# Kernel optimization log

Hardware: AMD Instinct MI355X
Metric: run time of the kernel (lower is better)

Reference implementation:

```python
import jax, jax.numpy as jnp
import numpy as np

H = 16
D_MODEL = 1024
D_K = D_MODEL // H


def setup_inputs() -> dict:
    key = jax.random.key(0)
    ks = jax.random.split(key, 12)
    B, S = 2, 2048
    scale = 1.0 / np.sqrt(D_MODEL)
    inp = {
        "query": jax.random.normal(ks[0], (B, S, D_MODEL), jnp.float32),
        "key": jax.random.normal(ks[1], (B, S, D_MODEL), jnp.float32),
        "value": jax.random.normal(ks[2], (B, S, D_MODEL), jnp.float32),
        "mask": jax.random.randint(ks[3], (B, S, S), 0, 2, jnp.int32),
        "w_q": jax.random.normal(ks[4], (D_MODEL, D_MODEL), jnp.float32) * scale,
        "b_q": jnp.zeros((D_MODEL,), jnp.float32),
        "w_k": jax.random.normal(ks[5], (D_MODEL, D_MODEL), jnp.float32) * scale,
        "b_k": jnp.zeros((D_MODEL,), jnp.float32),
        "w_v": jax.random.normal(ks[6], (D_MODEL, D_MODEL), jnp.float32) * scale,
        "b_v": jnp.zeros((D_MODEL,), jnp.float32),
        "w_o": jax.random.normal(ks[7], (D_MODEL, D_MODEL), jnp.float32) * scale,
        "b_o": jnp.zeros((D_MODEL,), jnp.float32),
    }
    return inp


def reference(query, key, value, mask, w_q, b_q, w_k, b_k, w_v, b_v, w_o, b_o):
    B, S, _ = query.shape
    # linear projections (torch nn.Linear: x @ W^T + b)
    q = query @ w_q.T + b_q
    k = key @ w_k.T + b_k
    v = value @ w_v.T + b_v
    # split heads -> [B, H, S, D_K]
    q = q.reshape(B, S, H, D_K).transpose(0, 2, 1, 3)
    k = k.reshape(B, S, H, D_K).transpose(0, 2, 1, 3)
    v = v.reshape(B, S, H, D_K).transpose(0, 2, 1, 3)
    # scores [B, H, S, S]; original masks BEFORE dividing by sqrt(d_k)
    scores = jnp.einsum("bhqd,bhkd->bhqk", q, k)
    m = mask[:, None, :, :]  # broadcast over heads (mask.unsqueeze(1))
    scores = jnp.where(m == 0, jnp.float32(-1e9), scores)
    scores = scores / jnp.sqrt(jnp.float32(D_K))
    attn = jax.nn.softmax(scores, axis=-1)
    # dropout is identity in eval mode
    ctx = jnp.einsum("bhqk,bhkd->bhqd", attn, v)
    ctx = ctx.transpose(0, 2, 1, 3).reshape(B, S, H * D_K)
    return ctx @ w_o.T + b_o
```

## Files before the change

kernel.cpp:

```cpp
#include <hip/hip_runtime.h>
#include <hip/hip_bf16.h>
#include <stdint.h>

typedef __attribute__((ext_vector_type(8))) short short8;
typedef __attribute__((ext_vector_type(4))) short short4v;
typedef __attribute__((ext_vector_type(4))) float f32x4;
typedef __attribute__((ext_vector_type(4))) unsigned short us4;
typedef unsigned short ushort_t;

#define LDS_AS __attribute__((address_space(3)))
#define GLB_AS __attribute__((address_space(1)))

__device__ __forceinline__ void gload_lds16(const void* g, void* l) {
    __builtin_amdgcn_global_load_lds((const GLB_AS uint32_t*)g, (LDS_AS uint32_t*)l, 16, 0, 0);
}

__device__ __forceinline__ unsigned short f2bf(float f) {
    union { float f; uint32_t u; } v; v.f = f;
    uint32_t r = v.u + 0x7FFFu + ((v.u >> 16) & 1u);
    return (unsigned short)(r >> 16);
}

__device__ __forceinline__ float fexp2(float x) {
#if __has_builtin(__builtin_amdgcn_exp2f)
    return __builtin_amdgcn_exp2f(x);
#else
    return exp2f(x);
#endif
}

__device__ __forceinline__ uint32_t fbits(float f) {
    union { float f; uint32_t u; } v; v.f = f; return v.u;
}

__device__ __forceinline__ f32x4 mfma32(short8 a, short8 b, f32x4 c) {
    return __builtin_amdgcn_mfma_f32_16x16x32_bf16(a, b, c, 0, 0, 0);
}
__device__ __forceinline__ f32x4 mfma16(short4v a, short4v b, f32x4 c) {
    return __builtin_amdgcn_mfma_f32_16x16x16bf16_1k(a, b, c, 0, 0, 0);
}

__device__ __forceinline__ short8 lds_frag(const char* base, int row, int kc) {
    int byte = row * 128 + ((kc ^ (row & 7)) << 4);
    return *(const short8*)(base + byte);
}

__global__ __launch_bounds__(256) void cvt_all(
    const float* p0, const float* p1, const float* p2, const float* p3,
    const float* p4, const float* p5, const float* p6,
    ushort_t* o0, ushort_t* o1, ushort_t* o2, ushort_t* o3,
    ushort_t* o4, ushort_t* o5, ushort_t* o6) {
    int z = blockIdx.y;
    const float* in = z == 0 ? p0 : z == 1 ? p1 : z == 2 ? p2 : z == 3 ? p3 : z == 4 ? p4 : z == 5 ? p5 : p6;
    ushort_t* out = z == 0 ? o0 : z == 1 ? o1 : z == 2 ? o2 : z == 3 ? o3 : z == 4 ? o4 : z == 5 ? o5 : o6;
    int n4 = z < 3 ? 1048576 : 262144;
    int i = blockIdx.x * 256 + threadIdx.x;
    int stride = gridDim.x * 256;
    for (; i < n4; i += stride) {
        float4 f = ((const float4*)in)[i];
        us4 o;
        o[0] = f2bf(f.x); o[1] = f2bf(f.y); o[2] = f2bf(f.z); o[3] = f2bf(f.w);
        ((us4*)out)[i] = o;
    }
}

__global__ __launch_bounds__(256) void pack_mask(const int* __restrict__ mask,
                                                 unsigned long long* __restrict__ out) {
    int i = blockIdx.x * 256 + threadIdx.x;
    unsigned long long bits = __ballot(mask[i] != 0);
    if ((threadIdx.x & 63) == 0) {
        int k = i & 2047, q = (i >> 11) & 2047, b = i >> 22;
        out[((size_t)b * 32 + (k >> 6)) * 2048 + q] = bits;
    }
}

__device__ __forceinline__ void gemm_core(const ushort_t* Ab, const ushort_t* Wb,
                                          char* ldsA, char* ldsW, int tid, f32x4 acc[4][4]) {
    constexpr int K = 1024;
    int lane = tid & 63, wid = tid >> 6;
    int cl = lane & 15, gr = lane >> 4;
    int wm = (wid >> 1) * 64, wn = (wid & 1) * 64;
#pragma unroll
    for (int i = 0; i < 4; ++i)
#pragma unroll
        for (int j = 0; j < 4; ++j) acc[i][j] = (f32x4)0.0f;

    for (int kt = 0; kt < K / 64; ++kt) {
        int k0 = kt * 64;
#pragma unroll
        for (int iss = 0; iss < 4; ++iss) {
            int c = iss * 256 + tid;
            int r = c >> 3, kc = (c & 7) ^ (r & 7);
            gload_lds16(Ab + (size_t)r * K + k0 + kc * 8, ldsA + c * 16);
            gload_lds16(Wb + (size_t)r * K + k0 + kc * 8, ldsW + c * 16);
        }
        __syncthreads();
#pragma unroll
        for (int ks = 0; ks < 2; ++ks) {
            short8 af[4], wf[4];
#pragma unroll
            for (int t = 0; t < 4; ++t) {
                af[t] = lds_frag(ldsA, wm + t * 16 + cl, ks * 4 + gr);
                wf[t] = lds_frag(ldsW, wn + t * 16 + cl, ks * 4 + gr);
            }
#pragma unroll
            for (int i = 0; i < 4; ++i)
#pragma unroll
                for (int j = 0; j < 4; ++j)
                    acc[i][j] = mfma32(af[i], wf[j], acc[i][j]);
        }
        __syncthreads();
    }
}

__global__ __launch_bounds__(256)
void gemm3(const ushort_t* A0, const ushort_t* A1, const ushort_t* A2,
           const ushort_t* W0, const ushort_t* W1, const ushort_t* W2,
           const float* B0, const float* B1, const float* B2,
           void* O0, void* O1, void* O2, int mode_ovr, float scl0) {
    __shared__ char lds[32768];
    char* ldsA = lds;
    char* ldsW = lds + 16384;
    int z = blockIdx.z;
    const ushort_t* A = z == 0 ? A0 : z == 1 ? A1 : A2;
    const ushort_t* W = z == 0 ? W0 : z == 1 ? W1 : W2;
    const float* bias = z == 0 ? B0 : z == 1 ? B1 : B2;
    void* out = z == 0 ? O0 : z == 1 ? O1 : O2;
    int mode = mode_ovr >= 0 ? mode_ovr : (z == 2 ? 1 : 0);
    float scl = z == 0 ? scl0 : 1.0f;

    int tid = threadIdx.x, lane = tid & 63, wid = tid >> 6;
    int cl = lane & 15, gr = lane >> 4;
    int wm = (wid >> 1) * 64, wn = (wid & 1) * 64;
    int bm = blockIdx.y * 128, bn = blockIdx.x * 128;

    f32x4 acc[4][4];
    gemm_core(A + (size_t)bm * 1024, W + (size_t)bn * 1024, ldsA, ldsW, tid, acc);

#pragma unroll
    for (int j = 0; j < 4; ++j) {
        int n = bn + wn + j * 16 + cl;
        float bv = bias[n];
#pragma unroll
        for (int i = 0; i < 4; ++i) {
            int mbase = bm + wm + i * 16 + gr * 4;
            if (mode == 0) {
#pragma unroll
                for (int r = 0; r < 4; ++r) {
                    int m = mbase + r;
                    float v = (acc[i][j][r] + bv) * scl;
                    size_t idx = (((size_t)((m >> 11) * 16 + (n >> 6))) * 2048 + (m & 2047)) * 64 + (n & 63);
                    ((ushort_t*)out)[idx] = f2bf(v);
                }
            } else if (mode == 1) {
                us4 pk;
#pragma unroll
                for (int r = 0; r < 4; ++r) pk[r] = f2bf(acc[i][j][r] + bv);
                size_t idx = (((size_t)((mbase >> 11) * 16 + (n >> 6))) * 64 + (n & 63)) * 2048 + (mbase & 2047);
                *(us4*)((ushort_t*)out + idx) = pk;
            } else {
#pragma unroll
                for (int r = 0; r < 4; ++r)
                    ((float*)out)[(size_t)(mbase + r) * 1024 + n] = acc[i][j][r] + bv;
            }
        }
    }
}

__global__ __launch_bounds__(512, 4)
void attn(const ushort_t* __restrict__ Q, const ushort_t* __restrict__ Kh,
          const ushort_t* __restrict__ Vt, const unsigned long long* __restrict__ PM,
          ushort_t* __restrict__ ctx) {
    constexpr int S = 2048;
    __shared__ char lds[65536];
    int tid = threadIdx.x, lane = tid & 63, wid = tid >> 6;
    int cl = lane & 15, gr = lane >> 4, c7 = cl & 7;
    int h2 = wid & 1;
    int qg = wid >> 1;

    int blk = (blockIdx.x & 7) * 64 + (blockIdx.x >> 3);
    int bh = blk >> 4, qt = blk & 15;
    int b = bh >> 4, h = bh & 15;
    const ushort_t* Qb = Q + (size_t)bh * S * 64;
    const ushort_t* Kb = Kh + (size_t)bh * S * 64;
    const ushort_t* Vb = Vt + (size_t)bh * 64 * S;
    int q0w = qt * 128 + qg * 32;

    short8 qreg[2][2];
#pragma unroll
    for (int qf = 0; qf < 2; ++qf)
#pragma unroll
        for (int ks = 0; ks < 2; ++ks)
            qreg[qf][ks] = *(const short8*)(Qb + (size_t)(q0w + qf * 16 + cl) * 64 + ks * 32 + gr * 8);

    f32x4 acc[2][4];
    f32x4 accl[2];
#pragma unroll
    for (int qf = 0; qf < 2; ++qf) {
        accl[qf] = (f32x4)0.0f;
#pragma unroll
        for (int df = 0; df < 4; ++df) acc[qf][df] = (f32x4)0.0f;
    }

    int hs = tid >> 8, stid = tid & 255;
    int kOff[2], vOff[2], dstL[2];
#pragma unroll
    for (int iss = 0; iss < 2; ++iss) {
        int L = iss * 256 + stid;
        int r = L >> 3, c = (L & 7) ^ (r & 7);
        kOff[iss] = r * 64 + c * 8;
        vOff[iss] = r * S + c * 8;
        dstL[iss] = L * 16;
    }
    char* sbase = lds + hs * 32768;

    int aK0 = cl * 128 + ((0 * 4 + gr) ^ c7) * 16;
    int aK1 = cl * 128 + ((1 * 4 + gr) ^ c7) * 16;
    int aV[4];
#pragma unroll
    for (int nf = 0; nf < 4; ++nf)
        aV[nf] = cl * 128 + (((2 * nf) + (gr >> 1)) ^ c7) * 16 + (gr & 1) * 8;

    const unsigned long long* pmq = PM + (size_t)b * 32 * 2048 + q0w + cl;

    short4v ones;
#pragma unroll
    for (int r = 0; r < 4; ++r) ones[r] = (short)0x3F80;

    auto stage = [&](int T, int parity) {
        const ushort_t* Ks = Kb + (size_t)T * 4096;
        const ushort_t* Vs = Vb + (size_t)T * 64;
        char* dst = sbase + parity * 16384;
#pragma unroll
        for (int iss = 0; iss < 2; ++iss) {
            gload_lds16(Ks + kOff[iss], dst + dstL[iss]);
            gload_lds16(Vs + vOff[iss], dst + 8192 + dstL[iss]);
        }
    };

    stage(hs * 16, 0);
    __syncthreads();

    char* mybase = lds + h2 * 32768;
    for (int t = 0; t < 16; ++t) {
        char* cb = mybase + (t & 1) * 16384;
        if (t < 15) stage(hs * 16 + t + 1, (t + 1) & 1);

        int kvi = h2 * 16 + t;
        unsigned long long w0 = pmq[(size_t)kvi * 2048];
        unsigned long long w1 = pmq[(size_t)kvi * 2048 + 16];

        f32x4 sc[2][4];
#pragma unroll
        for (int nf = 0; nf < 4; ++nf) {
            short8 k0 = *(const short8*)(cb + aK0 + nf * 2048);
            short8 k1 = *(const short8*)(cb + aK1 + nf * 2048);
#pragma unroll
            for (int qf = 0; qf < 2; ++qf) {
                f32x4 s = mfma32(k0, qreg[qf][0], (f32x4)0.0f);
                sc[qf][nf] = mfma32(k1, qreg[qf][1], s);
            }
        }

        short4v pk[2][4];
#pragma unroll
        for (int qf = 0; qf < 2; ++qf) {
            unsigned long long ws = (qf == 0 ? w0 : w1) >> (gr * 4);
            uint32_t lo = (uint32_t)ws, hi = (uint32_t)(ws >> 32);
#pragma unroll
            for (int nf = 0; nf < 4; ++nf) {
                uint32_t wb = nf < 2 ? lo : hi;
                uint32_t u[4];
#pragma unroll
                for (int r = 0; r < 4; ++r) {
                    uint32_t bit = wb & (1u << ((nf & 1) * 16 + r));
                    float sel = bit ? sc[qf][nf][r] : -1.0e9f;
                    u[r] = fbits(fexp2(sel)) + 0x8000u;
                }
                union { uint32_t d[2]; short4v v; } pp;
                pp.d[0] = __builtin_amdgcn_perm(u[1], u[0], 0x07060302u);
                pp.d[1] = __builtin_amdgcn_perm(u[3], u[2], 0x07060302u);
                pk[qf][nf] = pp.v;
            }
        }

#pragma unroll
        for (int nf = 0; nf < 4; ++nf) {
#pragma unroll
            for (int df = 0; df < 4; ++df) {
                short4v vf = *(const short4v*)(cb + 8192 + aV[nf] + df * 2048);
                acc[0][df] = mfma16(pk[0][nf], vf, acc[0][df]);
                acc[1][df] = mfma16(pk[1][nf], vf, acc[1][df]);
            }
            accl[0] = mfma16(pk[0][nf], ones, accl[0]);
            accl[1] = mfma16(pk[1][nf], ones, accl[1]);
        }
        __syncthreads();
    }

    if (h2) {
        float* dst = (float*)(lds + qg * 10240 + lane * 160);
#pragma unroll
        for (int qf = 0; qf < 2; ++qf) {
#pragma unroll
            for (int df = 0; df < 4; ++df)
                *(f32x4*)(dst + qf * 16 + df * 4) = acc[qf][df];
            *(f32x4*)(dst + 32 + qf * 4) = accl[qf];
        }
    }
    __syncthreads();
    if (!h2) {
        const float* src = (const float*)(lds + qg * 10240 + lane * 160);
#pragma unroll
        for (int qf = 0; qf < 2; ++qf) {
#pragma unroll
            for (int df = 0; df < 4; ++df)
                acc[qf][df] += *(const f32x4*)(src + qf * 16 + df * 4);
            accl[qf] += *(const f32x4*)(src + 32 + qf * 4);
        }
#pragma unroll
        for (int qf = 0; qf < 2; ++qf) {
            float inv[4];
#pragma unroll
            for (int r = 0; r < 4; ++r) inv[r] = 1.0f / accl[qf][r];
#pragma unroll
            for (int df = 0; df < 4; ++df)
#pragma unroll
                for (int r = 0; r < 4; ++r) {
                    int q = q0w + qf * 16 + gr * 4 + r;
                    int d = df * 16 + cl;
                    ctx[((size_t)b * S + q) * 1024 + h * 64 + d] = f2bf(acc[qf][df][r] * inv[r]);
                }
        }
    }
}

extern "C" void kernel_launch(void* const* d_in, const int* in_sizes, int n_in,
                              void* d_out, int out_size, void* d_ws, size_t ws_size,
                              hipStream_t stream) {
    const float* query = (const float*)d_in[0];
    const float* key   = (const float*)d_in[1];
    const float* value = (const float*)d_in[2];
    const int*   mask  = (const int*)d_in[3];
    const float* w_q = (const float*)d_in[4];
    const float* b_q = (const float*)d_in[5];
    const float* w_k = (const float*)d_in[6];
    const float* b_k = (const float*)d_in[7];
    const float* w_v = (const float*)d_in[8];
    const float* b_v = (const float*)d_in[9];
    const float* w_o = (const float*)d_in[10];
    const float* b_o = (const float*)d_in[11];

    char* ws = (char*)d_ws;
    const size_t MB = 1 << 20;
    ushort_t* xq  = (ushort_t*)(ws + 0 * MB);
    ushort_t* xk  = (ushort_t*)(ws + 8 * MB);
    ushort_t* xv  = (ushort_t*)(ws + 16 * MB);
    ushort_t* wq  = (ushort_t*)(ws + 24 * MB);
    ushort_t* wk  = (ushort_t*)(ws + 26 * MB);
    ushort_t* wv  = (ushort_t*)(ws + 28 * MB);
    ushort_t* wo  = (ushort_t*)(ws + 30 * MB);
    ushort_t* qhm = (ushort_t*)(ws + 32 * MB);
    ushort_t* khm = (ushort_t*)(ws + 40 * MB);
    ushort_t* vt  = (ushort_t*)(ws + 48 * MB);
    unsigned long long* pm = (unsigned long long*)(ws + 56 * MB);
    ushort_t* ctx = (ushort_t*)(ws + 0 * MB);

    const float QSCALE = 0.125f * 1.44269504088896f;

    cvt_all<<<dim3(1024, 7), 256, 0, stream>>>(query, key, value, w_q, w_k, w_v, w_o,
                                               xq, xk, xv, wq, wk, wv, wo);
    pack_mask<<<32768, 256, 0, stream>>>(mask, pm);

    gemm3<<<dim3(8, 32, 3), 256, 0, stream>>>(xq, xk, xv, wq, wk, wv, b_q, b_k, b_v,
                                              qhm, khm, vt, -1, QSCALE);

    attn<<<512, 512, 0, stream>>>(qhm, khm, vt, pm, ctx);

    gemm3<<<dim3(8, 32, 1), 256, 0, stream>>>(ctx, ctx, ctx, wo, wo, wo, b_o, b_o, b_o,
                                              d_out, d_out, d_out, 2, 1.0f);
}
```

Baseline: 160.4 us.

## Shrink GEMM M-tile to 64 rows, raise occupancy, remap workgroups across XCDs

Templates the projection GEMM on the M sub-tile count and launches it with 64x128 tiles instead of 128x128, which doubles the grid so more of the CUs have work. It also adds a launch_bounds occupancy hint and remaps block IDs so consecutive blocks land round-robin across the eight XCDs for better L2 locality. The cost is lower arithmetic intensity per tile, since the W tile is reloaded for half as many rows.

Result: faster. 150.3 us (-6.3%).

```diff
diff --git a/kernel.cpp b/kernel.cpp
--- a/kernel.cpp
+++ b/kernel.cpp
@@ -74,37 +74,44 @@
     }
 }
 
+template<int MI>
 __device__ __forceinline__ void gemm_core(const ushort_t* Ab, const ushort_t* Wb,
-                                          char* ldsA, char* ldsW, int tid, f32x4 acc[4][4]) {
+                                          char* ldsA, char* ldsW, int tid, f32x4 acc[MI][4]) {
     constexpr int K = 1024;
     int lane = tid & 63, wid = tid >> 6;
     int cl = lane & 15, gr = lane >> 4;
-    int wm = (wid >> 1) * 64, wn = (wid & 1) * 64;
-#pragma unroll
-    for (int i = 0; i < 4; ++i)
+    int wm = (wid >> 1) * (MI * 16), wn = (wid & 1) * 64;
+#pragma unroll
+    for (int i = 0; i < MI; ++i)
 #pragma unroll
         for (int j = 0; j < 4; ++j) acc[i][j] = (f32x4)0.0f;
 
     for (int kt = 0; kt < K / 64; ++kt) {
         int k0 = kt * 64;
+#pragma unroll
+        for (int iss = 0; iss < MI; ++iss) {
+            int c = iss * 256 + tid;
+            int r = c >> 3, kc = (c & 7) ^ (r & 7);
+            gload_lds16(Ab + (size_t)r * K + k0 + kc * 8, ldsA + c * 16);
+        }
 #pragma unroll
         for (int iss = 0; iss < 4; ++iss) {
             int c = iss * 256 + tid;
             int r = c >> 3, kc = (c & 7) ^ (r & 7);
-            gload_lds16(Ab + (size_t)r * K + k0 + kc * 8, ldsA + c * 16);
             gload_lds16(Wb + (size_t)r * K + k0 + kc * 8, ldsW + c * 16);
         }
         __syncthreads();
 #pragma unroll
         for (int ks = 0; ks < 2; ++ks) {
-            short8 af[4], wf[4];
-#pragma unroll
-            for (int t = 0; t < 4; ++t) {
+            short8 af[MI], wf[4];
+#pragma unroll
+            for (int t = 0; t < MI; ++t)
                 af[t] = lds_frag(ldsA, wm + t * 16 + cl, ks * 4 + gr);
+#pragma unroll
+            for (int t = 0; t < 4; ++t)
                 wf[t] = lds_frag(ldsW, wn + t * 16 + cl, ks * 4 + gr);
-            }
-#pragma unroll
-            for (int i = 0; i < 4; ++i)
+#pragma unroll
+            for (int i = 0; i < MI; ++i)
 #pragma unroll
                 for (int j = 0; j < 4; ++j)
                     acc[i][j] = mfma32(af[i], wf[j], acc[i][j]);
@@ -113,15 +120,25 @@
     }
 }
 
-__global__ __launch_bounds__(256)
+template<int MI>
+__global__ __launch_bounds__(256, 4)
 void gemm3(const ushort_t* A0, const ushort_t* A1, const ushort_t* A2,
            const ushort_t* W0, const ushort_t* W1, const ushort_t* W2,
            const float* B0, const float* B1, const float* B2,
            void* O0, void* O1, void* O2, int mode_ovr, float scl0) {
-    __shared__ char lds[32768];
+    __shared__ char lds[MI * 4096 + 16384];
     char* ldsA = lds;
-    char* ldsW = lds + 16384;
-    int z = blockIdx.z;
+    char* ldsW = lds + MI * 4096;
+
+    int gx = gridDim.x, gy = gridDim.y;
+    int nwg = gx * gy * gridDim.z;
+    int bid = blockIdx.x + gx * (blockIdx.y + gy * blockIdx.z);
+    int nb = (bid & 7) * (nwg >> 3) + (bid >> 3);
+    int bx = nb % gx;
+    int t2 = nb / gx;
+    int by = t2 % gy;
+    int z = t2 / gy;
+
     const ushort_t* A = z == 0 ? A0 : z == 1 ? A1 : A2;
     const ushort_t* W = z == 0 ? W0 : z == 1 ? W1 : W2;
     const float* bias = z == 0 ? B0 : z == 1 ? B1 : B2;
@@ -131,18 +148,18 @@
 
     int tid = threadIdx.x, lane = tid & 63, wid = tid >> 6;
     int cl = lane & 15, gr = lane >> 4;
-    int wm = (wid >> 1) * 64, wn = (wid & 1) * 64;
-    int bm = blockIdx.y * 128, bn = blockIdx.x * 128;
-
-    f32x4 acc[4][4];
-    gemm_core(A + (size_t)bm * 1024, W + (size_t)bn * 1024, ldsA, ldsW, tid, acc);
+    int wm = (wid >> 1) * (MI * 16), wn = (wid & 1) * 64;
+    int bm = by * (MI * 32), bn = bx * 128;
+
+    f32x4 acc[MI][4];
+    gemm_core<MI>(A + (size_t)bm * 1024, W + (size_t)bn * 1024, ldsA, ldsW, tid, acc);
 
 #pragma unroll
     for (int j = 0; j < 4; ++j) {
         int n = bn + wn + j * 16 + cl;
         float bv = bias[n];
 #pragma unroll
-        for (int i = 0; i < 4; ++i) {
+        for (int i = 0; i < MI; ++i) {
             int mbase = bm + wm + i * 16 + gr * 4;
             if (mode == 0) {
 #pragma unroll
@@ -372,11 +389,11 @@
                                                xq, xk, xv, wq, wk, wv, wo);
     pack_mask<<<32768, 256, 0, stream>>>(mask, pm);
 
-    gemm3<<<dim3(8, 32, 3), 256, 0, stream>>>(xq, xk, xv, wq, wk, wv, b_q, b_k, b_v,
-                                              qhm, khm, vt, -1, QSCALE);
+    gemm3<2><<<dim3(8, 64, 3), 256, 0, stream>>>(xq, xk, xv, wq, wk, wv, b_q, b_k, b_v,
+                                                 qhm, khm, vt, -1, QSCALE);
 
     attn<<<512, 512, 0, stream>>>(qhm, khm, vt, pm, ctx);
 
-    gemm3<<<dim3(8, 32, 1), 256, 0, stream>>>(ctx, ctx, ctx, wo, wo, wo, b_o, b_o, b_o,
-                                              d_out, d_out, d_out, 2, 1.0f);
-}
+    gemm3<2><<<dim3(8, 64, 1), 256, 0, stream>>>(ctx, ctx, ctx, wo, wo, wo, b_o, b_o, b_o,
+                                                 d_out, d_out, d_out, 2, 1.0f);
+}
```
